# Performance work log

Hardware: AMD Instinct MI355X
Metric: run time of the kernel (lower is better)

## Reference

```python
import jax, jax.numpy as jnp
import numpy as np

B = 512       # batch
N = 64        # max_nodes
H = 256       # hidden_dim
LAT = 128     # latent_dim
HEADS = 4
HC = H // HEADS   # per-head channels (GATConv out_channels)
NF = 64       # node_features
L = 3         # num_dec_layers
R = 8         # lora_r
SCAL = 16.0 / R   # lora_alpha / r
NB = 4        # num_bond_types
SLOPE = 0.2   # GATConv leaky_relu negative slope


def setup_inputs() -> dict:
    key = jax.random.key(0)
    ks = jax.random.split(key, 21)
    f = lambda k, shape, s=0.05: jax.random.normal(k, shape, dtype=jnp.float32) * s
    Din = H + LAT  # GAT input dim = hidden + latent (concat)
    return {
        "z": jax.random.normal(ks[0], (B, LAT), dtype=jnp.float32),
        # z_to_nodes LoRALinear: latent -> hidden*max_nodes
        "z2n_w": f(ks[1], (H * N, LAT)), "z2n_b": f(ks[2], (H * N,)),
        "z2n_A": f(ks[3], (R, LAT)), "z2n_B": f(ks[4], (H * N, R)),
        # GATConv stacks (same Din every layer): lin weight, att_src, att_dst, bias
        "gat_W": f(ks[5], (L, HEADS * HC, Din)),
        "gat_asrc": f(ks[6], (L, HEADS, HC)),
        "gat_adst": f(ks[7], (L, HEADS, HC)),
        "gat_bias": f(ks[8], (L, H)),
        # node predictor LoRALinear: hidden -> node_features
        "node_w": f(ks[9], (NF, H)), "node_b": f(ks[10], (NF,)),
        "node_A": f(ks[11], (R, H)), "node_B": f(ks[12], (NF, R)),
        # adj predictor LoRALinear: 2*hidden -> 1
        "adj_w": f(ks[13], (1, 2 * H)), "adj_b": f(ks[14], (1,)),
        "adj_A": f(ks[15], (R, 2 * H)), "adj_B": f(ks[16], (1, R)),
        # bond type predictor LoRALinear: 2*hidden -> 4
        "bond_w": f(ks[17], (NB, 2 * H)), "bond_b": f(ks[18], (NB,)),
        "bond_A": f(ks[19], (R, 2 * H)), "bond_B": f(ks[20], (NB, R)),
    }


def _lora_w(W, A, Bm):
    # effective weight of LoRALinear (eval mode, dropout off): W + (alpha/r) * B @ A
    return W + SCAL * (Bm @ A)


def _forward(z, z2n_w, z2n_b, z2n_A, z2n_B, gat_W, gat_asrc, gat_adst, gat_bias,
             node_w, node_b, node_A, node_B, adj_w, adj_b, adj_A, adj_B,
             bond_w, bond_b, bond_A, bond_B):
    # z_to_nodes: LoRA linear + ReLU -> [B, N, H]
    x = jax.nn.relu(z @ _lora_w(z2n_w, z2n_A, z2n_B).T + z2n_b).reshape(B, N, H)
    z_bc = jnp.broadcast_to(z[:, None, :], (B, N, LAT))
    # Fully-connected graph (off-diagonal edges) + GATConv default self loops
    # => dense softmax attention over all N source nodes per target, per graph.
    for l in range(L):
        xc = jnp.concatenate([x, z_bc], axis=-1)                      # [B,N,H+LAT]
        Wr = gat_W[l].reshape(HEADS, HC, H + LAT)
        h = jnp.einsum('bnd,hcd->bnhc', xc, Wr)                        # [B,N,heads,HC]
        e_src = jnp.einsum('bnhc,hc->bnh', h, gat_asrc[l])             # source term
        e_dst = jnp.einsum('bnhc,hc->bnh', h, gat_adst[l])             # target term
        e = e_dst[:, :, None, :] + e_src[:, None, :, :]                # [B,i,j,heads]
        e = jnp.where(e > 0, e, SLOPE * e)                             # leaky_relu
        alpha = jax.nn.softmax(e, axis=2)                              # over sources j
        out = jnp.einsum('bijh,bjhc->bihc', alpha, h).reshape(B, N, H) + gat_bias[l]
        x = jax.nn.relu(out)
    # node reconstruction
    recon_nodes = x @ _lora_w(node_w, node_A, node_B).T + node_b       # [B,N,NF]
    # pairwise predictors: Linear(concat[h_i,h_j]) = W1 h_i + W2 h_j + b
    iu = jnp.triu(jnp.ones((N, N), dtype=bool), 1)
    Wa = _lora_w(adj_w, adj_A, adj_B)                                  # [1,2H]
    s1 = x @ Wa[:, :H].T                                               # [B,N,1]
    s2 = x @ Wa[:, H:].T
    Am = s1 + jnp.swapaxes(s2, 1, 2) + adj_b[0]                        # Am[i,j]=s1[i]+s2[j]
    adj_logits = jnp.where(iu, Am, jnp.where(iu.T, jnp.swapaxes(Am, 1, 2), 0.0))
    Wb = _lora_w(bond_w, bond_A, bond_B)                               # [NB,2H]
    t1 = x @ Wb[:, :H].T                                               # [B,N,NB]
    t2 = x @ Wb[:, H:].T
    Bm = t1[:, :, None, :] + t2[:, None, :, :] + bond_b                # [B,N,N,NB]
    bond_logits = jnp.where(iu[:, :, None], Bm,
                            jnp.where(iu.T[:, :, None], jnp.swapaxes(Bm, 1, 2), 0.0))
    return recon_nodes, adj_logits, bond_logits


def reference(z, z2n_w, z2n_b, z2n_A, z2n_B, gat_W, gat_asrc, gat_adst, gat_bias,
              node_w, node_b, node_A, node_B, adj_w, adj_b, adj_A, adj_B,
              bond_w, bond_b, bond_A, bond_B):
    return _forward(z, z2n_w, z2n_b, z2n_A, z2n_B, gat_W, gat_asrc, gat_adst, gat_bias,
                    node_w, node_b, node_A, node_B, adj_w, adj_b, adj_A, adj_B,
                    bond_w, bond_b, bond_A, bond_B)
```

## Files before the change

kernel.cpp:

```cpp
#include <hip/hip_runtime.h>


typedef float float4v __attribute__((ext_vector_type(4)));
typedef short short8v __attribute__((ext_vector_type(8)));

struct alignas(8) us4 { ushort x, y, z, w; };

#define ZA_OFF 0UL
#define HZ_OFF 4096UL
#define EZ_OFF 397312UL
#define XBF_U   819200UL
#define ZBF_U   9207808UL
#define GWBF_U  9273344UL
#define WZBF_U  9568256UL
#define PW_U    11665408UL
#define WST_U   11759616UL

__device__ inline ushort f2bf(float f) {
    uint u = __float_as_uint(f);
    uint r = (u + 0x7FFFu + ((u >> 16) & 1u)) >> 16;
    return (ushort)r;
}
__device__ inline float bf2f(ushort u) { return __uint_as_float(((uint)u) << 16); }

__device__ inline int xidx(int r, int cu) {
    int ch = cu >> 3;
    return r * 256 + (((ch ^ (r & 7))) << 3) + (cu & 7);
}

struct P3 { short8v b0, b1, b2; };
__device__ inline P3 loadP3(const ushort* pw, int lo, int hi, int kk) {
    P3 f;
    f.b0 = *(const short8v*)(pw + (size_t)(      lo)*256 + kk*32 + hi*8);
    f.b1 = *(const short8v*)(pw + (size_t)(16  + lo)*256 + kk*32 + hi*8);
    f.b2 = *(const short8v*)(pw + (size_t)(32  + lo)*256 + kk*32 + hi*8);
    return f;
}
struct P2 { short8v b3, b4; };
__device__ inline P2 loadP2(const ushort* pw, int lo, int hi, int kk) {
    P2 f;
    f.b3 = *(const short8v*)(pw + (size_t)(48 + lo)*256 + kk*32 + hi*8);
    f.b4 = *(const short8v*)(pw + (size_t)(64 + lo)*256 + kk*32 + hi*8);
    return f;
}

__device__ inline void stage3(ushort* dst, const ushort* src, int w, int ln) {
    int c0 = w * 512, c1 = (w + 8) * 512;
    __builtin_amdgcn_global_load_lds(
        (const __attribute__((address_space(1))) void*)(src + c0 + ln*8),
        (__attribute__((address_space(3))) void*)(dst + c0), 16, 0, 0);
    __builtin_amdgcn_global_load_lds(
        (const __attribute__((address_space(1))) void*)(src + c1 + ln*8),
        (__attribute__((address_space(3))) void*)(dst + c1), 16, 0, 0);
    if (w < 4) {
        int c2 = (w + 16) * 512;
        __builtin_amdgcn_global_load_lds(
            (const __attribute__((address_space(1))) void*)(src + c2 + ln*8),
            (__attribute__((address_space(3))) void*)(dst + c2), 16, 0, 0);
    }
}

__global__ __launch_bounds__(256) void k_setup(
    const float* __restrict__ z, const float* __restrict__ z2nA,
    const float* __restrict__ nodeW, const float* __restrict__ nodeA, const float* __restrict__ nodeB,
    const float* __restrict__ adjW, const float* __restrict__ adjA, const float* __restrict__ adjB,
    const float* __restrict__ bondW, const float* __restrict__ bondA, const float* __restrict__ bondB,
    const float* __restrict__ gatW, const float* __restrict__ z2nw,
    const float* __restrict__ asrcp, const float* __restrict__ adstp,
    float* __restrict__ wsf)
{
    ushort* wsu = (ushort*)wsf;
    int gid = blockIdx.x * 256 + threadIdx.x;
    if (gid < 4096) {
        int b = gid >> 3, r = gid & 7;
        const float* zp = z + (size_t)b * 128;
        const float* ap = z2nA + (size_t)r * 128;
        float s = 0.f;
        #pragma unroll 8
        for (int k = 0; k < 128; ++k) s += zp[k] * ap[k];
        wsf[ZA_OFF + gid] = s;
    } else if (gid < 24576) {
        int idx = gid - 4096;
        int r = idx >> 8, c = idx & 255;
        float v = 0.f;
        if (r < 64) {
            float s = 0.f;
            #pragma unroll
            for (int k = 0; k < 8; ++k) s += nodeB[r*8+k] * nodeA[k*256+c];
            v = nodeW[r*256+c] + 2.0f * s;
        } else if (r < 66) {
            int off = (r - 64) * 256 + c;
            float s = 0.f;
            #pragma unroll
            for (int k = 0; k < 8; ++k) s += adjB[k] * adjA[k*512+off];
            v = adjW[off] + 2.0f * s;
        } else if (r < 70) {
            int q = r - 66;
            float s = 0.f;
            #pragma unroll
            for (int k = 0; k < 8; ++k) s += bondB[q*8+k] * bondA[k*512+c];
            v = bondW[q*512+c] + 2.0f * s;
        } else if (r < 74) {
            int q = r - 70;
            float s = 0.f;
            #pragma unroll
            for (int k = 0; k < 8; ++k) s += bondB[q*8+k] * bondA[k*512+256+c];
            v = bondW[q*512+256+c] + 2.0f * s;
        }
        wsu[PW_U + idx] = f2bf(v);
    } else if (gid < 55296) {
        int idx = gid - 24576;
        int lkk = idx / 1280;
        int rem = idx - lkk * 1280;
        int head = rem / 320;
        int rem2 = rem - head * 320;
        int frag = rem2 >> 6;
        int ln = rem2 & 63;
        int lo = ln & 15, hi = ln >> 4;
        int l = lkk >> 3, kk = lkk & 7;
        ushort* dst = wsu + WST_U + (size_t)idx * 8;
        if (frag < 4) {
            const float* srcw = gatW + ((size_t)(l*256 + head*64 + frag*16 + lo))*384 + kk*32 + hi*8;
            #pragma unroll
            for (int j = 0; j < 8; ++j) dst[j] = f2bf(srcw[j]);
        } else {
            float s[8] = {0.f,0.f,0.f,0.f,0.f,0.f,0.f,0.f};
            if (lo < 2) {
                const float* av = (lo == 0 ? asrcp : adstp) + l*256 + head*64;
                const float* wp = gatW + ((size_t)(l*256 + head*64))*384 + kk*32 + hi*8;
                for (int hc = 0; hc < 64; ++hc) {
                    float a = av[hc];
                    const float* wr = wp + (size_t)hc * 384;
                    #pragma unroll
                    for (int j = 0; j < 8; ++j) s[j] += wr[j] * a;
                }
            }
            #pragma unroll
            for (int j = 0; j < 8; ++j) dst[j] = f2bf(s[j]);
        }
    } else {
        int cid = gid - 55296;
        const float* src; ushort* dst; int idx;
        if (cid < 16384)        { src = z;     dst = wsu + ZBF_U;  idx = cid; }
        else if (cid < 90112)   { src = gatW;  dst = wsu + GWBF_U; idx = cid - 16384; }
        else if (cid < 614400)  { src = z2nw;  dst = wsu + WZBF_U; idx = cid - 90112; }
        else return;
        float4 v = ((const float4*)src)[idx];
        us4 o; o.x = f2bf(v.x); o.y = f2bf(v.y); o.z = f2bf(v.z); o.w = f2bf(v.w);
        ((us4*)dst)[idx] = o;
    }
}

__global__ __launch_bounds__(256) void k_hz(
    const float* __restrict__ asrcp, const float* __restrict__ adstp,
    float* __restrict__ wsf)
{
    ushort* wsu = (ushort*)wsf;
    int t = threadIdx.x;
    int w = t >> 6, ln = t & 63, lo = ln & 15, hi = ln >> 4;
    int l = blockIdx.x >> 3, bg = blockIdx.x & 7;
    const ushort* wz = wsu + GWBF_U + (size_t)l * 98304;
    const ushort* zb = wsu + ZBF_U + (size_t)bg * 64 * 128;
    float4v acc[4][4];
    #pragma unroll
    for (int m = 0; m < 4; ++m)
        #pragma unroll
        for (int n = 0; n < 4; ++n) acc[m][n] = (float4v)(0.f);
    #pragma unroll
    for (int kk = 0; kk < 4; ++kk) {
        short8v a[4], bq[4];
        #pragma unroll
        for (int m = 0; m < 4; ++m)
            a[m] = *(const short8v*)(wz + (size_t)(w*64 + m*16 + lo)*384 + 256 + kk*32 + hi*8);
        #pragma unroll
        for (int n = 0; n < 4; ++n)
            bq[n] = *(const short8v*)(zb + (size_t)(n*16 + lo)*128 + kk*32 + hi*8);
        #pragma unroll
        for (int m = 0; m < 4; ++m)
            #pragma unroll
            for (int n = 0; n < 4; ++n)
                acc[m][n] = __builtin_amdgcn_mfma_f32_16x16x32_bf16(a[m], bq[n], acc[m][n], 0, 0, 0);
    }
    float* hzp = wsf + HZ_OFF + (size_t)l * 131072;
    #pragma unroll
    for (int m = 0; m < 4; ++m)
        #pragma unroll
        for (int n = 0; n < 4; ++n)
            #pragma unroll
            for (int q = 0; q < 4; ++q)
                hzp[(size_t)(bg*64 + n*16 + lo)*256 + w*64 + m*16 + hi*4 + q] = acc[m][n][q];
    float as_[4][4], ad_[4][4];
    #pragma unroll
    for (int m = 0; m < 4; ++m)
        #pragma unroll
        for (int q = 0; q < 4; ++q) {
            as_[m][q] = asrcp[l*256 + w*64 + m*16 + hi*4 + q];
            ad_[m][q] = adstp[l*256 + w*64 + m*16 + hi*4 + q];
        }
    #pragma unroll
    for (int n = 0; n < 4; ++n) {
        float ss = 0.f, dd = 0.f;
        #pragma unroll
        for (int m = 0; m < 4; ++m)
            #pragma unroll
            for (int q = 0; q < 4; ++q) {
                ss += acc[m][n][q] * as_[m][q];
                dd += acc[m][n][q] * ad_[m][q];
            }
        ss += __shfl_xor(ss, 16); ss += __shfl_xor(ss, 32);
        dd += __shfl_xor(dd, 16); dd += __shfl_xor(dd, 32);
        if (hi == 0) {
            int b = bg*64 + n*16 + lo;
            wsf[EZ_OFF + (size_t)(l*2 + 0)*2048 + (size_t)b*4 + w] = ss;
            wsf[EZ_OFF + (size_t)(l*2 + 1)*2048 + (size_t)b*4 + w] = dd;
        }
    }
}

__global__ __launch_bounds__(256) void k_z2n(
    const float* __restrict__ bias, const float* __restrict__ lB,
    float* __restrict__ wsf)
{
    ushort* wsu = (ushort*)wsf;
    int t = threadIdx.x;
    int w = t >> 6, ln = t & 63, lo = ln & 15, hi = ln >> 4;
    int bm = blockIdx.x >> 6, bn = blockIdx.x & 63;
    int brow0 = bm * 64;
    int o0 = bn * 256 + w * 64;
    const ushort* wz = wsu + WZBF_U;
    const ushort* zb = wsu + ZBF_U;
    float4v acc[4][4];
    #pragma unroll
    for (int m = 0; m < 4; ++m)
        #pragma unroll
        for (int n = 0; n < 4; ++n) acc[m][n] = (float4v)(0.f);
    #pragma unroll
    for (int kk = 0; kk < 4; ++kk) {
        short8v a[4], bq[4];
        #pragma unroll
        for (int m = 0; m < 4; ++m)
            a[m] = *(const short8v*)(wz + (size_t)(o0 + m*16 + lo)*128 + kk*32 + hi*8);
        #pragma unroll
        for (int n = 0; n < 4; ++n)
            bq[n] = *(const short8v*)(zb + (size_t)(brow0 + n*16 + lo)*128 + kk*32 + hi*8);
        #pragma unroll
        for (int m = 0; m < 4; ++m)
            #pragma unroll
            for (int n = 0; n < 4; ++n)
                acc[m][n] = __builtin_amdgcn_mfma_f32_16x16x32_bf16(a[m], bq[n], acc[m][n], 0, 0, 0);
    }
    const float* zA = wsf + ZA_OFF;
    float4 za0[4], za1[4];
    #pragma unroll
    for (int n = 0; n < 4; ++n) {
        int brow = brow0 + n*16 + lo;
        za0[n] = *(const float4*)&zA[brow*8];
        za1[n] = *(const float4*)&zA[brow*8 + 4];
    }
    #pragma unroll
    for (int m = 0; m < 4; ++m) {
        float lor[4][4]; float bs[4];
        #pragma unroll
        for (int q = 0; q < 4; ++q) {
            int o = o0 + m*16 + hi*4 + q;
            float4 b20 = *(const float4*)&lB[(size_t)o*8];
            float4 b21 = *(const float4*)&lB[(size_t)o*8 + 4];
            bs[q] = bias[o];
            #pragma unroll
            for (int n = 0; n < 4; ++n)
                lor[n][q] = za0[n].x*b20.x + za0[n].y*b20.y + za0[n].z*b20.z + za0[n].w*b20.w
                          + za1[n].x*b21.x + za1[n].y*b21.y + za1[n].z*b21.z + za1[n].w*b21.w;
        }
        #pragma unroll
        for (int n = 0; n < 4; ++n) {
            int brow = brow0 + n*16 + lo;
            float v0 = acc[m][n][0] + 2.f*lor[n][0] + bs[0]; v0 = v0 > 0.f ? v0 : 0.f;
            float v1 = acc[m][n][1] + 2.f*lor[n][1] + bs[1]; v1 = v1 > 0.f ? v1 : 0.f;
            float v2 = acc[m][n][2] + 2.f*lor[n][2] + bs[2]; v2 = v2 > 0.f ? v2 : 0.f;
            float v3 = acc[m][n][3] + 2.f*lor[n][3] + bs[3]; v3 = v3 > 0.f ? v3 : 0.f;
            us4 pk; pk.x = f2bf(v0); pk.y = f2bf(v1); pk.z = f2bf(v2); pk.w = f2bf(v3);
            *(us4*)(wsu + XBF_U + (size_t)brow*16384 + o0 + m*16 + hi*4) = pk;
        }
    }
}

__global__ __launch_bounds__(512, 4) void k_fused(
    const float* __restrict__ gbias,
    const float* __restrict__ nodeb, const float* __restrict__ adjb,
    const float* __restrict__ bondb,
    float* __restrict__ wsf, float* __restrict__ out)
{
    extern __shared__ ushort dyn[];
    ushort* Rr   = dyn;
    ushort* bbuf = dyn + 17408;
    float*  scr  = (float*)(dyn + 17408 + 20480);
    ushort* wsu = (ushort*)wsf;
    int t = threadIdx.x;
    int w = t >> 6, ln = t & 63, lo = ln & 15, hi = ln >> 4;
    int head = w & 3, m0 = (w >> 2) * 32;
    int b = blockIdx.x;
    const ushort* xb = wsu + XBF_U + (size_t)b * 16384;

    #pragma unroll
    for (int i = 0; i < 4; ++i) {
        int flat = i*512 + t;
        int r = flat >> 5, ch = flat & 31;
        short8v v = *(const short8v*)(xb + (size_t)r*256 + ch*8);
        *(short8v*)&Rr[r*256 + ((ch ^ (r & 7)) << 3)] = v;
    }
    __syncthreads();

    float* es = scr;
    float* ed = scr + 256;

    for (int l = 0; l < 3; ++l) {
        const ushort* wst = wsu + WST_U + (size_t)l * 81920;
        const float*  hzp = wsf + HZ_OFF + (size_t)l*131072 + (size_t)b*256 + head*64;

        float hz0 = hzp[lo], hz1 = hzp[16 + lo], hz2 = hzp[32 + lo], hz3 = hzp[48 + lo];
        float ezs = wsf[EZ_OFF + (size_t)(l*2 + 0)*2048 + (size_t)b*4 + head];
        float ezd = wsf[EZ_OFF + (size_t)(l*2 + 1)*2048 + (size_t)b*4 + head];

        stage3(bbuf, wst, w, ln);

        float4v acc[2][4], accE[2];
        float eInit = (lo == 0) ? ezs : (lo == 1 ? ezd : 0.f);
        accE[0] = (float4v)(eInit); accE[1] = (float4v)(eInit);
        acc[0][0] = (float4v)(hz0); acc[1][0] = (float4v)(hz0);
        acc[0][1] = (float4v)(hz1); acc[1][1] = (float4v)(hz1);
        acc[0][2] = (float4v)(hz2); acc[1][2] = (float4v)(hz2);
        acc[0][3] = (float4v)(hz3); acc[1][3] = (float4v)(hz3);

        for (int kk = 0; kk < 8; ++kk) {
            __syncthreads();
            if (kk < 7)
                stage3(bbuf + ((kk+1)&1)*10240, wst + (size_t)(kk+1)*10240, w, ln);
            const ushort* bb = bbuf + (kk&1)*10240 + head*2560;
            short8v bq0 = *(const short8v*)(bb +        ln*8);
            short8v bq1 = *(const short8v*)(bb +  512 + ln*8);
            short8v bq2 = *(const short8v*)(bb + 1024 + ln*8);
            short8v bq3 = *(const short8v*)(bb + 1536 + ln*8);
            short8v bsd = *(const short8v*)(bb + 2048 + ln*8);
            short8v a0 = *(const short8v*)&Rr[xidx(m0 + lo,      kk*32 + hi*8)];
            short8v a1 = *(const short8v*)&Rr[xidx(m0 + 16 + lo, kk*32 + hi*8)];
            acc[0][0] = __builtin_amdgcn_mfma_f32_16x16x32_bf16(a0, bq0, acc[0][0], 0, 0, 0);
            acc[1][0] = __builtin_amdgcn_mfma_f32_16x16x32_bf16(a1, bq0, acc[1][0], 0, 0, 0);
            acc[0][1] = __builtin_amdgcn_mfma_f32_16x16x32_bf16(a0, bq1, acc[0][1], 0, 0, 0);
            acc[1][1] = __builtin_amdgcn_mfma_f32_16x16x32_bf16(a1, bq1, acc[1][1], 0, 0, 0);
            acc[0][2] = __builtin_amdgcn_mfma_f32_16x16x32_bf16(a0, bq2, acc[0][2], 0, 0, 0);
            acc[1][2] = __builtin_amdgcn_mfma_f32_16x16x32_bf16(a1, bq2, acc[1][2], 0, 0, 0);
            acc[0][3] = __builtin_amdgcn_mfma_f32_16x16x32_bf16(a0, bq3, acc[0][3], 0, 0, 0);
            acc[1][3] = __builtin_amdgcn_mfma_f32_16x16x32_bf16(a1, bq3, acc[1][3], 0, 0, 0);
            accE[0]   = __builtin_amdgcn_mfma_f32_16x16x32_bf16(a0, bsd, accE[0], 0, 0, 0);
            accE[1]   = __builtin_amdgcn_mfma_f32_16x16x32_bf16(a1, bsd, accE[1], 0, 0, 0);
        }
        if (lo == 0) {
            *(float4*)&es[head*64 + m0 + hi*4]      = make_float4(accE[0][0], accE[0][1], accE[0][2], accE[0][3]);
            *(float4*)&es[head*64 + m0 + 16 + hi*4] = make_float4(accE[1][0], accE[1][1], accE[1][2], accE[1][3]);
        } else if (lo == 1) {
            *(float4*)&ed[head*64 + m0 + hi*4]      = make_float4(accE[0][0], accE[0][1], accE[0][2], accE[0][3]);
            *(float4*)&ed[head*64 + m0 + 16 + hi*4] = make_float4(accE[1][0], accE[1][1], accE[1][2], accE[1][3]);
        }

        __syncthreads();

        #pragma unroll
        for (int m = 0; m < 2; ++m)
            #pragma unroll
            for (int n = 0; n < 4; ++n) {
                us4 pk;
                pk.x = f2bf(acc[m][n][0]); pk.y = f2bf(acc[m][n][1]);
                pk.z = f2bf(acc[m][n][2]); pk.w = f2bf(acc[m][n][3]);
                *(us4*)&Rr[head*4352 + (n*16 + lo)*68 + m0 + m*16 + hi*4] = pk;
            }

        __syncthreads();

        float4v acc2[4][2];
        #pragma unroll
        for (int m = 0; m < 4; ++m)
            #pragma unroll
            for (int n = 0; n < 2; ++n) acc2[m][n] = (float4v)(0.f);
        float psum[2] = {0.f, 0.f};
        #pragma unroll
        for (int kk = 0; kk < 2; ++kk) {
            short8v hb[4];
            #pragma unroll
            for (int m = 0; m < 4; ++m)
                hb[m] = *(const short8v*)&Rr[head*4352 + (m*16 + lo)*68 + kk*32 + hi*8];
            float4 e0 = *(const float4*)&es[head*64 + kk*32 + hi*8];
            float4 e1 = *(const float4*)&es[head*64 + kk*32 + hi*8 + 4];
            float ej[8] = {e0.x, e0.y, e0.z, e0.w, e1.x, e1.y, e1.z, e1.w};
            #pragma unroll
            for (int n = 0; n < 2; ++n) {
                float edr = ed[head*64 + m0 + n*16 + lo];
                short8v af; float pp = 0.f;
                #pragma unroll
                for (int jj = 0; jj < 8; ++jj) {
                    float e = edr + ej[jj];
                    e = fmaxf(e, 0.2f * e);
                    float p = __expf(e);
                    pp += p;
                    af[jj] = (short)f2bf(p);
                }
                psum[n] += pp;
                #pragma unroll
                for (int m = 0; m < 4; ++m)
                    acc2[m][n] = __builtin_amdgcn_mfma_f32_16x16x32_bf16(hb[m], af, acc2[m][n], 0, 0, 0);
            }
        }
        float rs[2];
        #pragma unroll
        for (int n = 0; n < 2; ++n) {
            psum[n] += __shfl_xor(psum[n], 16);
            psum[n] += __shfl_xor(psum[n], 32);
            rs[n] = 1.0f / psum[n];
        }

        __syncthreads();

        #pragma unroll
        for (int m = 0; m < 4; ++m) {
            int c0 = head*64 + m*16 + hi*4;
            float b0f = gbias[l*256 + c0 + 0];
            float b1f = gbias[l*256 + c0 + 1];
            float b2f = gbias[l*256 + c0 + 2];
            float b3f = gbias[l*256 + c0 + 3];
            #pragma unroll
            for (int n = 0; n < 2; ++n) {
                int r = m0 + n*16 + lo;
                float v0 = acc2[m][n][0]*rs[n] + b0f; v0 = v0 > 0.f ? v0 : 0.f;
                float v1 = acc2[m][n][1]*rs[n] + b1f; v1 = v1 > 0.f ? v1 : 0.f;
                float v2 = acc2[m][n][2]*rs[n] + b2f; v2 = v2 > 0.f ? v2 : 0.f;
                float v3 = acc2[m][n][3]*rs[n] + b3f; v3 = v3 > 0.f ? v3 : 0.f;
                us4 pk; pk.x = f2bf(v0); pk.y = f2bf(v1); pk.z = f2bf(v2); pk.w = f2bf(v3);
                *(us4*)&Rr[xidx(r, c0)] = pk;
            }
        }

        __syncthreads();
    }

    const ushort* pw = wsu + PW_U;
    int pq = w & 3, pn = w >> 2;
    if (pn == 0) {
        float4v p0 = (float4v)(0.f), p1 = (float4v)(0.f), p2 = (float4v)(0.f);
        P3 fA = loadP3(pw, lo, hi, 0);
        #pragma unroll
        for (int ii = 0; ii < 4; ++ii) {
            P3 fB = loadP3(pw, lo, hi, 2*ii + 1);
            {
                int kk = 2*ii;
                short8v a = *(const short8v*)&Rr[xidx(pq*16 + lo, kk*32 + hi*8)];
                p0 = __builtin_amdgcn_mfma_f32_16x16x32_bf16(a, fA.b0, p0, 0, 0, 0);
                p1 = __builtin_amdgcn_mfma_f32_16x16x32_bf16(a, fA.b1, p1, 0, 0, 0);
                p2 = __builtin_amdgcn_mfma_f32_16x16x32_bf16(a, fA.b2, p2, 0, 0, 0);
            }
            if (ii < 3) fA = loadP3(pw, lo, hi, 2*ii + 2);
            {
                int kk = 2*ii + 1;
                short8v a = *(const short8v*)&Rr[xidx(pq*16 + lo, kk*32 + hi*8)];
                p0 = __builtin_amdgcn_mfma_f32_16x16x32_bf16(a, fB.b0, p0, 0, 0, 0);
                p1 = __builtin_amdgcn_mfma_f32_16x16x32_bf16(a, fB.b1, p1, 0, 0, 0);
                p2 = __builtin_amdgcn_mfma_f32_16x16x32_bf16(a, fB.b2, p2, 0, 0, 0);
            }
        }
        __syncthreads();
        float* Rf = (float*)Rr;
        #pragma unroll
        for (int qq = 0; qq < 4; ++qq) {
            int nd = pq*16 + hi*4 + qq;
            Rf[nd*68 + lo]      = p0[qq];
            Rf[nd*68 + 16 + lo] = p1[qq];
            Rf[nd*68 + 32 + lo] = p2[qq];
        }
    } else {
        float4v p3 = (float4v)(0.f), paux = (float4v)(0.f);
        P2 fA = loadP2(pw, lo, hi, 0);
        #pragma unroll
        for (int ii = 0; ii < 4; ++ii) {
            P2 fB = loadP2(pw, lo, hi, 2*ii + 1);
            {
                int kk = 2*ii;
                short8v a = *(const short8v*)&Rr[xidx(pq*16 + lo, kk*32 + hi*8)];
                p3   = __builtin_amdgcn_mfma_f32_16x16x32_bf16(a, fA.b3, p3, 0, 0, 0);
                paux = __builtin_amdgcn_mfma_f32_16x16x32_bf16(a, fA.b4, paux, 0, 0, 0);
            }
            if (ii < 3) fA = loadP2(pw, lo, hi, 2*ii + 2);
            {
                int kk = 2*ii + 1;
                short8v a = *(const short8v*)&Rr[xidx(pq*16 + lo, kk*32 + hi*8)];
                p3   = __builtin_amdgcn_mfma_f32_16x16x32_bf16(a, fB.b3, p3, 0, 0, 0);
                paux = __builtin_amdgcn_mfma_f32_16x16x32_bf16(a, fB.b4, paux, 0, 0, 0);
            }
        }
        __syncthreads();
        float* Rf = (float*)Rr;
        #pragma unroll
        for (int qq = 0; qq < 4; ++qq) {
            int nd = pq*16 + hi*4 + qq;
            Rf[nd*68 + 48 + lo] = p3[qq];
            float v = paux[qq];
            if (lo == 0)      scr[nd] = v;
            else if (lo == 1) scr[64 + nd] = v;
            else if (lo < 6)  scr[128 + nd*5 + (lo-2)] = v;
            else if (lo < 10) scr[448 + nd*5 + (lo-6)] = v;
        }
    }
    __syncthreads();

    {
        const float* Rf = (const float*)Rr;
        #pragma unroll
        for (int it = 0; it < 2; ++it) {
            int idx = it*512 + t;
            int nd = idx >> 4, f0 = (idx & 15) * 4;
            float4 v = *(const float4*)&Rf[nd*68 + f0];
            float4 bv = *(const float4*)&nodeb[f0];
            v.x += bv.x; v.y += bv.y; v.z += bv.z; v.w += bv.w;
            *(float4*)&out[(size_t)b*4096 + (size_t)idx*4] = v;
        }
    }

    float ab = adjb[0];
    #pragma unroll
    for (int it = 0; it < 2; ++it) {
        int idx = it*512 + t;
        int flat = idx * 4;
        int i = flat >> 6, j0 = flat & 63;
        float4 v; float* vp = (float*)&v;
        #pragma unroll
        for (int uu = 0; uu < 4; ++uu) {
            int j = j0 + uu;
            float val;
            if (i == j)      val = 0.f;
            else if (i < j)  val = scr[i] + scr[64 + j] + ab;
            else             val = scr[j] + scr[64 + i] + ab;
            vp[uu] = val;
        }
        *(float4*)&out[2097152UL + (size_t)b*4096 + flat] = v;
    }

    float4 bb2 = *(const float4*)bondb;
    #pragma unroll
    for (int it = 0; it < 8; ++it) {
        int fl4 = it*512 + t;
        int i = fl4 >> 6, j = fl4 & 63;
        float4 v;
        if (i == j) { v.x = v.y = v.z = v.w = 0.f; }
        else {
            int a2 = i < j ? i : j, c2 = i < j ? j : i;
            v.x = scr[128 + a2*5 + 0] + scr[448 + c2*5 + 0] + bb2.x;
            v.y = scr[128 + a2*5 + 1] + scr[448 + c2*5 + 1] + bb2.y;
            v.z = scr[128 + a2*5 + 2] + scr[448 + c2*5 + 2] + bb2.z;
            v.w = scr[128 + a2*5 + 3] + scr[448 + c2*5 + 3] + bb2.w;
        }
        *(float4*)&out[4194304UL + (size_t)b*16384 + (size_t)fl4*4] = v;
    }
}

extern "C" void kernel_launch(void* const* d_in, const int* in_sizes, int n_in,
                              void* d_out, int out_size, void* d_ws, size_t ws_size,
                              hipStream_t stream)
{
    const float* z     = (const float*)d_in[0];
    const float* z2nw  = (const float*)d_in[1];
    const float* z2nb  = (const float*)d_in[2];
    const float* z2nA  = (const float*)d_in[3];
    const float* z2nB  = (const float*)d_in[4];
    const float* gatW  = (const float*)d_in[5];
    const float* asrc  = (const float*)d_in[6];
    const float* adst  = (const float*)d_in[7];
    const float* gbias = (const float*)d_in[8];
    const float* nodew = (const float*)d_in[9];
    const float* nodeb = (const float*)d_in[10];
    const float* nodeA = (const float*)d_in[11];
    const float* nodeB = (const float*)d_in[12];
    const float* adjw  = (const float*)d_in[13];
    const float* adjb  = (const float*)d_in[14];
    const float* adjA  = (const float*)d_in[15];
    const float* adjB  = (const float*)d_in[16];
    const float* bondw = (const float*)d_in[17];
    const float* bondb = (const float*)d_in[18];
    const float* bondA = (const float*)d_in[19];
    const float* bondB = (const float*)d_in[20];
    float* ws  = (float*)d_ws;
    float* out = (float*)d_out;

    k_setup<<<2616, 256, 0, stream>>>(z, z2nA, nodew, nodeA, nodeB,
                                      adjw, adjA, adjB, bondw, bondA, bondB,
                                      gatW, z2nw, asrc, adst, ws);
    k_hz<<<24, 256, 0, stream>>>(asrc, adst, ws);
    k_z2n<<<512, 256, 0, stream>>>(z2nb, z2nB, ws);
    k_fused<<<512, 512, 78848, stream>>>(gbias, nodeb, adjb, bondb, ws, out);
}
```

Before: 93.12 us.

## Repartition GAT projection per wave by head-half and drop per-k block barriers

The GAT linear projection loop is reorganised so that each wave owns one head and half of that head's output channels across all 64 nodes, instead of one head and half the nodes. Each wave now stages only the weight slices it consumes, using its own global_load_lds calls with a two-deep buffer. Readiness is tracked with per-wave vmcnt/lgkmcnt waits rather than a __syncthreads on every k step. This removes eight block-wide barriers per layer, but waves with c0h==1 idle while the c0h==0 waves run the extra attention-score MFMAs. The wave's A-operand loads from LDS also double, and correctness now depends on the hand-written waitcnt counts.

```diff
diff --git a/kernel.cpp b/kernel.cpp
--- a/kernel.cpp
+++ b/kernel.cpp
@@ -44,19 +44,20 @@
     return f;
 }
 
-__device__ inline void stage3(ushort* dst, const ushort* src, int w, int ln) {
-    int c0 = w * 512, c1 = (w + 8) * 512;
+__device__ inline void gll(const ushort* src, ushort* dst) {
     __builtin_amdgcn_global_load_lds(
-        (const __attribute__((address_space(1))) void*)(src + c0 + ln*8),
-        (__attribute__((address_space(3))) void*)(dst + c0), 16, 0, 0);
-    __builtin_amdgcn_global_load_lds(
-        (const __attribute__((address_space(1))) void*)(src + c1 + ln*8),
-        (__attribute__((address_space(3))) void*)(dst + c1), 16, 0, 0);
-    if (w < 4) {
-        int c2 = (w + 16) * 512;
-        __builtin_amdgcn_global_load_lds(
-            (const __attribute__((address_space(1))) void*)(src + c2 + ln*8),
-            (__attribute__((address_space(3))) void*)(dst + c2), 16, 0, 0);
+        (const __attribute__((address_space(1))) void*)src,
+        (__attribute__((address_space(3))) void*)dst, 16, 0, 0);
+}
+
+__device__ inline void stageW(ushort* dstHead, const ushort* srcHead, int c0h, int ln) {
+    if (c0h == 0) {
+        gll(srcHead +        ln*8, dstHead);
+        gll(srcHead +  512 + ln*8, dstHead + 512);
+        gll(srcHead + 2048 + ln*8, dstHead + 2048);
+    } else {
+        gll(srcHead + 1024 + ln*8, dstHead + 1024);
+        gll(srcHead + 1536 + ln*8, dstHead + 1536);
     }
 }
 
@@ -298,6 +299,7 @@
     int t = threadIdx.x;
     int w = t >> 6, ln = t & 63, lo = ln & 15, hi = ln >> 4;
     int head = w & 3, m0 = (w >> 2) * 32;
+    int headH = w >> 1, c0h = w & 1;
     int b = blockIdx.x;
     const ushort* xb = wsu + XBF_U + (size_t)b * 16384;
 
@@ -315,63 +317,91 @@
 
     for (int l = 0; l < 3; ++l) {
         const ushort* wst = wsu + WST_U + (size_t)l * 81920;
-        const float*  hzp = wsf + HZ_OFF + (size_t)l*131072 + (size_t)b*256 + head*64;
-
-        float hz0 = hzp[lo], hz1 = hzp[16 + lo], hz2 = hzp[32 + lo], hz3 = hzp[48 + lo];
-        float ezs = wsf[EZ_OFF + (size_t)(l*2 + 0)*2048 + (size_t)b*4 + head];
-        float ezd = wsf[EZ_OFF + (size_t)(l*2 + 1)*2048 + (size_t)b*4 + head];
-
-        stage3(bbuf, wst, w, ln);
-
-        float4v acc[2][4], accE[2];
+        const float*  hzp = wsf + HZ_OFF + (size_t)l*131072 + (size_t)b*256 + headH*64;
+
+        float hzA = hzp[(c0h*2    )*16 + lo];
+        float hzB = hzp[(c0h*2 + 1)*16 + lo];
+        float ezs = wsf[EZ_OFF + (size_t)(l*2 + 0)*2048 + (size_t)b*4 + headH];
+        float ezd = wsf[EZ_OFF + (size_t)(l*2 + 1)*2048 + (size_t)b*4 + headH];
+
+        float4v acc[2][4], accE[4];
         float eInit = (lo == 0) ? ezs : (lo == 1 ? ezd : 0.f);
-        accE[0] = (float4v)(eInit); accE[1] = (float4v)(eInit);
-        acc[0][0] = (float4v)(hz0); acc[1][0] = (float4v)(hz0);
-        acc[0][1] = (float4v)(hz1); acc[1][1] = (float4v)(hz1);
-        acc[0][2] = (float4v)(hz2); acc[1][2] = (float4v)(hz2);
-        acc[0][3] = (float4v)(hz3); acc[1][3] = (float4v)(hz3);
-
+        #pragma unroll
+        for (int m = 0; m < 4; ++m) {
+            acc[0][m] = (float4v)(hzA);
+            acc[1][m] = (float4v)(hzB);
+            accE[m]   = (float4v)(eInit);
+        }
+
+        asm volatile("s_waitcnt vmcnt(0)" ::: "memory");
+        __builtin_amdgcn_sched_barrier(0);
+        stageW(bbuf +         headH*2560, wst +         headH*2560, c0h, ln);
+        stageW(bbuf + 10240 + headH*2560, wst + 10240 + headH*2560, c0h, ln);
+
+        #pragma unroll
         for (int kk = 0; kk < 8; ++kk) {
-            __syncthreads();
-            if (kk < 7)
-                stage3(bbuf + ((kk+1)&1)*10240, wst + (size_t)(kk+1)*10240, w, ln);
-            const ushort* bb = bbuf + (kk&1)*10240 + head*2560;
-            short8v bq0 = *(const short8v*)(bb +        ln*8);
-            short8v bq1 = *(const short8v*)(bb +  512 + ln*8);
-            short8v bq2 = *(const short8v*)(bb + 1024 + ln*8);
-            short8v bq3 = *(const short8v*)(bb + 1536 + ln*8);
-            short8v bsd = *(const short8v*)(bb + 2048 + ln*8);
-            short8v a0 = *(const short8v*)&Rr[xidx(m0 + lo,      kk*32 + hi*8)];
-            short8v a1 = *(const short8v*)&Rr[xidx(m0 + 16 + lo, kk*32 + hi*8)];
+            if (kk < 7) {
+                if (c0h == 0) { asm volatile("s_waitcnt vmcnt(3)" ::: "memory"); }
+                else          { asm volatile("s_waitcnt vmcnt(2)" ::: "memory"); }
+            } else {
+                asm volatile("s_waitcnt vmcnt(0)" ::: "memory");
+            }
+            __builtin_amdgcn_sched_barrier(0);
+            const ushort* bb = bbuf + (kk&1)*10240 + headH*2560;
+            short8v bq0 = *(const short8v*)(bb + (c0h*2    )*512 + ln*8);
+            short8v bq1 = *(const short8v*)(bb + (c0h*2 + 1)*512 + ln*8);
+            short8v bsd = {};
+            if (c0h == 0) bsd = *(const short8v*)(bb + 2048 + ln*8);
+            short8v a0 = *(const short8v*)&Rr[xidx(     lo, kk*32 + hi*8)];
+            short8v a1 = *(const short8v*)&Rr[xidx(16 + lo, kk*32 + hi*8)];
+            short8v a2 = *(const short8v*)&Rr[xidx(32 + lo, kk*32 + hi*8)];
+            short8v a3 = *(const short8v*)&Rr[xidx(48 + lo, kk*32 + hi*8)];
+            if (kk < 6) {
+                asm volatile("s_waitcnt lgkmcnt(0)" ::: "memory");
+                __builtin_amdgcn_sched_barrier(0);
+                stageW(bbuf + (kk&1)*10240 + headH*2560,
+                       wst + (size_t)(kk+2)*10240 + headH*2560, c0h, ln);
+            }
             acc[0][0] = __builtin_amdgcn_mfma_f32_16x16x32_bf16(a0, bq0, acc[0][0], 0, 0, 0);
-            acc[1][0] = __builtin_amdgcn_mfma_f32_16x16x32_bf16(a1, bq0, acc[1][0], 0, 0, 0);
-            acc[0][1] = __builtin_amdgcn_mfma_f32_16x16x32_bf16(a0, bq1, acc[0][1], 0, 0, 0);
+            acc[0][1] = __builtin_amdgcn_mfma_f32_16x16x32_bf16(a1, bq0, acc[0][1], 0, 0, 0);
+            acc[0][2] = __builtin_amdgcn_mfma_f32_16x16x32_bf16(a2, bq0, acc[0][2], 0, 0, 0);
+            acc[0][3] = __builtin_amdgcn_mfma_f32_16x16x32_bf16(a3, bq0, acc[0][3], 0, 0, 0);
+            acc[1][0] = __builtin_amdgcn_mfma_f32_16x16x32_bf16(a0, bq1, acc[1][0], 0, 0, 0);
             acc[1][1] = __builtin_amdgcn_mfma_f32_16x16x32_bf16(a1, bq1, acc[1][1], 0, 0, 0);
-            acc[0][2] = __builtin_amdgcn_mfma_f32_16x16x32_bf16(a0, bq2, acc[0][2], 0, 0, 0);
-            acc[1][2] = __builtin_amdgcn_mfma_f32_16x16x32_bf16(a1, bq2, acc[1][2], 0, 0, 0);
-            acc[0][3] = __builtin_amdgcn_mfma_f32_16x16x32_bf16(a0, bq3, acc[0][3], 0, 0, 0);
-            acc[1][3] = __builtin_amdgcn_mfma_f32_16x16x32_bf16(a1, bq3, acc[1][3], 0, 0, 0);
-            accE[0]   = __builtin_amdgcn_mfma_f32_16x16x32_bf16(a0, bsd, accE[0], 0, 0, 0);
-            accE[1]   = __builtin_amdgcn_mfma_f32_16x16x32_bf16(a1, bsd, accE[1], 0, 0, 0);
-        }
-        if (lo == 0) {
-            *(float4*)&es[head*64 + m0 + hi*4]      = make_float4(accE[0][0], accE[0][1], accE[0][2], accE[0][3]);
-            *(float4*)&es[head*64 + m0 + 16 + hi*4] = make_float4(accE[1][0], accE[1][1], accE[1][2], accE[1][3]);
-        } else if (lo == 1) {
-            *(float4*)&ed[head*64 + m0 + hi*4]      = make_float4(accE[0][0], accE[0][1], accE[0][2], accE[0][3]);
-            *(float4*)&ed[head*64 + m0 + 16 + hi*4] = make_float4(accE[1][0], accE[1][1], accE[1][2], accE[1][3]);
+            acc[1][2] = __builtin_amdgcn_mfma_f32_16x16x32_bf16(a2, bq1, acc[1][2], 0, 0, 0);
+            acc[1][3] = __builtin_amdgcn_mfma_f32_16x16x32_bf16(a3, bq1, acc[1][3], 0, 0, 0);
+            if (c0h == 0) {
+                accE[0] = __builtin_amdgcn_mfma_f32_16x16x32_bf16(a0, bsd, accE[0], 0, 0, 0);
+                accE[1] = __builtin_amdgcn_mfma_f32_16x16x32_bf16(a1, bsd, accE[1], 0, 0, 0);
+                accE[2] = __builtin_amdgcn_mfma_f32_16x16x32_bf16(a2, bsd, accE[2], 0, 0, 0);
+                accE[3] = __builtin_amdgcn_mfma_f32_16x16x32_bf16(a3, bsd, accE[3], 0, 0, 0);
+            }
+        }
+
+        if (c0h == 0) {
+            if (lo == 0) {
+                #pragma unroll
+                for (int m = 0; m < 4; ++m)
+                    *(float4*)&es[headH*64 + m*16 + hi*4] =
+                        make_float4(accE[m][0], accE[m][1], accE[m][2], accE[m][3]);
+            } else if (lo == 1) {
+                #pragma unroll
+                for (int m = 0; m < 4; ++m)
+                    *(float4*)&ed[headH*64 + m*16 + hi*4] =
+                        make_float4(accE[m][0], accE[m][1], accE[m][2], accE[m][3]);
+            }
         }
 
         __syncthreads();
 
         #pragma unroll
-        for (int m = 0; m < 2; ++m)
-            #pragma unroll
-            for (int n = 0; n < 4; ++n) {
+        for (int cf = 0; cf < 2; ++cf)
+            #pragma unroll
+            for (int m = 0; m < 4; ++m) {
                 us4 pk;
-                pk.x = f2bf(acc[m][n][0]); pk.y = f2bf(acc[m][n][1]);
-                pk.z = f2bf(acc[m][n][2]); pk.w = f2bf(acc[m][n][3]);
-                *(us4*)&Rr[head*4352 + (n*16 + lo)*68 + m0 + m*16 + hi*4] = pk;
+                pk.x = f2bf(acc[cf][m][0]); pk.y = f2bf(acc[cf][m][1]);
+                pk.z = f2bf(acc[cf][m][2]); pk.w = f2bf(acc[cf][m][3]);
+                *(us4*)&Rr[headH*4352 + ((c0h*2 + cf)*16 + lo)*68 + m*16 + hi*4] = pk;
             }
 
         __syncthreads();
```

New measurement: 92.57 us. No clear change (-0.6%).
